# Performance work log

Hardware: AMD Instinct MI355X
Metric: run time of the kernel (lower is better)

Reference implementation:

```python
import math
import jax, jax.numpy as jnp
import numpy as np
from jax import lax

# FPN anchor layout: 1024x768 image, strides {4,8,16,32,64}, 3 anchors/location
NUM_PER_LEVEL = (147456, 36864, 9216, 2304, 576)
A_TOTAL = sum(NUM_PER_LEVEL)
BATCH = 8
PRE_NMS_TOP_N = 1000   # testing
POST_NMS_TOP_N = 1000  # testing
NMS_THRESH = 0.7
SCORE_THRESH = 0.0
MIN_SIZE = 1.0
IMG_H, IMG_W = 768.0, 1024.0
BBOX_XFORM_CLIP = math.log(1000.0 / 16.0)


def setup_inputs() -> dict:
    key = jax.random.key(0)
    k1, k2, k3, k4, k5, k6 = jax.random.split(key, 6)
    objectness = jax.random.normal(k1, (BATCH, A_TOTAL), jnp.float32)
    pred_bbox_deltas = jax.random.normal(k2, (BATCH, A_TOTAL, 4), jnp.float32) * 0.2
    # valid anchor boxes (x1, y1, x2, y2)
    cx = jax.random.uniform(k3, (A_TOTAL,), jnp.float32) * IMG_W
    cy = jax.random.uniform(k4, (A_TOTAL,), jnp.float32) * IMG_H
    w = 16.0 + jax.random.uniform(k5, (A_TOTAL,), jnp.float32) * 176.0
    h = 16.0 + jax.random.uniform(k6, (A_TOTAL,), jnp.float32) * 176.0
    anchors = jnp.stack([cx - 0.5 * w, cy - 0.5 * h, cx + 0.5 * w, cy + 0.5 * h], -1)
    return {"objectness": objectness, "pred_bbox_deltas": pred_bbox_deltas, "anchors": anchors}


def _nms_image(boxes, scores, lvl, valid):
    """batched_nms (level-offset trick) + post-NMS top-k, fixed shapes.
    boxes [K,4], scores [K], lvl [K] int, valid [K] bool -> [POST_NMS_TOP_N, 5]"""
    K = boxes.shape[0]
    s = jnp.where(valid, scores, -1.0)
    order = jnp.argsort(-s)  # decreasing score (invalid last)
    b = boxes[order]
    s = s[order]
    v = valid[order]
    # offset boxes per level so cross-level boxes never overlap (torchvision batched_nms)
    offset = lvl[order].astype(b.dtype) * (jnp.max(lax.stop_gradient(boxes)) + 1.0)
    nb = lax.stop_gradient(b) + offset[:, None]
    area = (nb[:, 2] - nb[:, 0]) * (nb[:, 3] - nb[:, 1])
    lt = jnp.maximum(nb[:, None, :2], nb[None, :, :2])  # [K,K,2]
    rb = jnp.minimum(nb[:, None, 2:], nb[None, :, 2:])
    wh = jnp.clip(rb - lt, 0.0)
    inter = wh[..., 0] * wh[..., 1]
    iou = inter / jnp.maximum(area[:, None] + area[None, :] - inter, 1e-9)
    pos = jnp.arange(K)

    def body(keep, i):
        sup = keep[i] & (iou[i] > NMS_THRESH) & (pos > i)
        return keep & ~sup, None

    keep, _ = lax.scan(body, v, pos)
    masked = jnp.where(keep, s, -1.0)
    top_s, top_i = lax.top_k(masked, POST_NMS_TOP_N)  # kept, decreasing score
    sel_b = b[top_i]
    ok = top_s > -0.5
    sel_b = jnp.where(ok[:, None], sel_b, 0.0)
    top_s = jnp.where(ok, top_s, 0.0)
    return jnp.concatenate([sel_b, top_s[:, None]], axis=-1)


def reference(objectness, pred_bbox_deltas, anchors):
    # --- box decode (BoxCoder, weights (1,1,1,1)) ---
    wa = anchors[:, 2] - anchors[:, 0]
    ha = anchors[:, 3] - anchors[:, 1]
    cxa = anchors[:, 0] + 0.5 * wa
    cya = anchors[:, 1] + 0.5 * ha
    dx, dy = pred_bbox_deltas[..., 0], pred_bbox_deltas[..., 1]
    dw = jnp.minimum(pred_bbox_deltas[..., 2], BBOX_XFORM_CLIP)
    dh = jnp.minimum(pred_bbox_deltas[..., 3], BBOX_XFORM_CLIP)
    pcx = dx * wa + cxa
    pcy = dy * ha + cya
    pw = jnp.exp(dw) * wa
    ph = jnp.exp(dh) * ha
    proposals = jnp.stack(
        [pcx - 0.5 * pw, pcy - 0.5 * ph, pcx + 0.5 * pw, pcy + 0.5 * ph], axis=-1
    )  # [B, A, 4]

    # --- per-level pre-NMS top-k (_get_top_n_idx) ---
    levels = jnp.concatenate(
        [jnp.full((n,), i, jnp.int32) for i, n in enumerate(NUM_PER_LEVEL)]
    )
    idx_parts = []
    off = 0
    for n in NUM_PER_LEVEL:
        k = min(PRE_NMS_TOP_N, n)
        _, ti = lax.top_k(objectness[:, off:off + n], k)
        idx_parts.append(ti + off)
        off += n
    top_idx = jnp.concatenate(idx_parts, axis=1)  # [B, K]

    scores = jax.nn.sigmoid(jnp.take_along_axis(objectness, top_idx, axis=1))
    lvl = levels[top_idx]
    boxes = jnp.take_along_axis(proposals, top_idx[..., None], axis=1)  # [B,K,4]

    # --- clip to image ---
    x1 = jnp.clip(boxes[..., 0], 0.0, IMG_W)
    y1 = jnp.clip(boxes[..., 1], 0.0, IMG_H)
    x2 = jnp.clip(boxes[..., 2], 0.0, IMG_W)
    y2 = jnp.clip(boxes[..., 3], 0.0, IMG_H)
    boxes = jnp.stack([x1, y1, x2, y2], axis=-1)

    # remove_small_boxes + score threshold (as validity mask; fixed shapes)
    valid = ((x2 - x1) >= MIN_SIZE) & ((y2 - y1) >= MIN_SIZE) & (scores >= SCORE_THRESH)

    # --- per-image batched NMS + post-NMS top-k ---
    return jax.vmap(_nms_image)(boxes, scores, lvl, valid)  # [B, POST_NMS_TOP_N, 5]
```

## Files before the change

kernel.cpp:

```cpp
#include <hip/hip_runtime.h>
#include <math.h>

#pragma clang fp contract(off)

#define A_TOTAL 196416
#define BATCH 8
#define KTOT 4576
#define NLEV 5
#define MSPLIT 16
#define RCAP 6144
#define NPARTS 24

static __device__ const int d_aoff[NLEV] = {0, 147456, 184320, 193536, 195840};
static __device__ const int d_n[NLEV]    = {147456, 36864, 9216, 2304, 576};
static __device__ const int d_k[NLEV]    = {1000, 1000, 1000, 1000, 576};
static __device__ const int d_spl[NLEV]  = {8, 2, 1, 1, 1};
static __device__ const int d_bp[NLEV]   = {0, 8, 10, 11, 12};
static __device__ const int d_pb_l[13]    = {0,0,0,0,0,0,0,0,1,1,2,3,4};
static __device__ const int d_pb_part[13] = {0,1,2,3,4,5,6,7,0,1,0,0,0};

#define TM_IOU (0.699999988079071044921875 + 0x1p-25)

__device__ inline unsigned int mono(float f) {
  unsigned int u = __float_as_uint(f);
  return (u & 0x80000000u) ? ~u : (u | 0x80000000u);
}
__device__ inline float imono(unsigned int m) {
  return __uint_as_float((m & 0x80000000u) ? (m & 0x7FFFFFFFu) : ~m);
}

__device__ inline int cnt_gt(const float* A, int n, float s) {
  int lo = 0, hi = n;
  while (lo < hi) { int mid = (lo + hi) >> 1; if (A[mid] > s) lo = mid + 1; else hi = mid; }
  return lo;
}
__device__ inline int cnt_ge(const float* A, int n, float s) {
  int lo = 0, hi = n;
  while (lo < hi) { int mid = (lo + hi) >> 1; if (A[mid] >= s) lo = mid + 1; else hi = mid; }
  return lo;
}

__global__ __launch_bounds__(1024) void k_hist(const float* __restrict__ obj,
                                               int* __restrict__ hist_g,
                                               int* __restrict__ cnt_g,
                                               float* __restrict__ maxblk) {
  int blk = blockIdx.x;
  int tid = threadIdx.x;
  if (blk == 0) {
    for (int i = tid; i < 40 * NPARTS; i += 1024) maxblk[i] = 0.0f;
    for (int i = tid; i < 40; i += 1024) cnt_g[i] = 0;
  }
  int b = blk / 13, pb = blk % 13;
  int l = d_pb_l[pb], part = d_pb_part[pb];
  int slice = d_n[l] / d_spl[l];
  int start = d_aoff[l] + part * slice;
  const float4* p4 = (const float4*)(obj + (size_t)b * A_TOTAL + start);
  int s4 = slice >> 2;
  __shared__ int h[4096];
  for (int i = tid; i < 4096; i += 1024) h[i] = 0;
  __syncthreads();
  for (int i = tid; i < s4; i += 1024) {
    float4 v = p4[i];
    atomicAdd(&h[mono(v.x) >> 20], 1);
    atomicAdd(&h[mono(v.y) >> 20], 1);
    atomicAdd(&h[mono(v.z) >> 20], 1);
    atomicAdd(&h[mono(v.w) >> 20], 1);
  }
  __syncthreads();
  int* outp = hist_g + (size_t)blk * 4096;
  for (int i = tid; i < 4096; i += 1024) outp[i] = h[i];
}

__global__ __launch_bounds__(1024) void k_collect(const float* __restrict__ obj,
                                                  const int* __restrict__ hist_g,
                                                  int* __restrict__ cnt_g,
                                                  unsigned long long* __restrict__ cand_g) {
  int blk = blockIdx.x;
  int b = blk / 13, pb = blk % 13;
  int l = d_pb_l[pb], part = d_pb_part[pb];
  int bl = b * NLEV + l;
  const int k = d_k[l];
  int tid = threadIdx.x;
  __shared__ int t[4096];
  __shared__ int grp[256];
  __shared__ unsigned int sP;
  __shared__ __align__(16) unsigned long long lbuf[RCAP];
  __shared__ int s_cnt, s_base;
  int parts = d_spl[l];
  const int* hb = hist_g + (size_t)(b * 13 + d_bp[l]) * 4096;
  for (int bin = tid; bin < 4096; bin += 1024) {
    int s = 0;
    for (int p = 0; p < parts; ++p) s += hb[p * 4096 + bin];
    t[bin] = s;
  }
  if (tid == 0) s_cnt = 0;
  __syncthreads();
  if (tid < 256) {
    int s = 0;
    for (int j = 0; j < 16; ++j) s += t[tid * 16 + j];
    grp[tid] = s;
  }
  __syncthreads();
  if (tid == 0) {
    int cum = 0, g, d;
    for (g = 255; g >= 0; --g) {
      if (cum + grp[g] >= k) break;
      cum += grp[g];
    }
    for (d = 15; d >= 0; --d) {
      int c = t[g * 16 + d];
      if (cum + c >= k) break;
      cum += c;
    }
    sP = (unsigned int)(g * 16 + d);
  }
  __syncthreads();
  unsigned int P = sP;
  int slice = d_n[l] / parts;
  int start = d_aoff[l] + part * slice;
  const float4* p4 = (const float4*)(obj + (size_t)b * A_TOTAL + start);
  int s4 = slice >> 2;
  int lbase = part * slice;
  for (int i = tid; i < s4; i += 1024) {
    float4 v = p4[i];
    unsigned int a[4] = {mono(v.x), mono(v.y), mono(v.z), mono(v.w)};
#pragma unroll
    for (int c = 0; c < 4; ++c) {
      if ((a[c] >> 20) >= P) {
        int slot = atomicAdd(&s_cnt, 1);
        if (slot < RCAP) {
          int idx = lbase + 4 * i + c;
          lbuf[slot] = ((unsigned long long)a[c] << 32) |
                       (unsigned int)(~(unsigned int)idx);
        }
      }
    }
  }
  __syncthreads();
  int cnt = min(s_cnt, RCAP);
  if (tid == 0) s_base = atomicAdd(&cnt_g[bl], cnt);
  __syncthreads();
  int base = s_base;
  for (int i = tid; i < cnt; i += 1024) {
    int slot = base + i;
    if (slot < RCAP) cand_g[(size_t)bl * RCAP + slot] = lbuf[i];
  }
}

__global__ __launch_bounds__(256) void k_rankdec(const unsigned long long* __restrict__ cand_g,
                                                 const int* __restrict__ cnt_g,
                                                 const float* __restrict__ deltas,
                                                 const float* __restrict__ anchors,
                                                 float* __restrict__ sc0,
                                                 float4* __restrict__ box0,
                                                 float* __restrict__ maxblk) {
  int bl = blockIdx.x / NPARTS, part = blockIdx.x % NPARTS;
  int b = bl / NLEV, l = bl % NLEV;
  const int k = d_k[l], aoff = d_aoff[l];
  int cnt = min(cnt_g[bl], RCAP);
  if (part * 256 >= cnt) return;
  __shared__ __align__(16) unsigned long long cb[RCAP];
  __shared__ unsigned int s_max;
  int tid = threadIdx.x;
  if (tid == 0) s_max = 0u;
  const unsigned long long* src = cand_g + (size_t)bl * RCAP;
  for (int i = tid; i < cnt; i += 256) cb[i] = src[i];
  __syncthreads();
  int myi = part * 256 + tid;
  float mx = 0.0f;
  if (myi < cnt) {
    unsigned long long e = cb[myi];
    int rank = 0;
    int nc2 = cnt >> 1;
    const ulonglong2* c2 = (const ulonglong2*)cb;
    for (int j = 0; j < nc2; ++j) {
      ulonglong2 v = c2[j];
      rank += (v.x > e) + (v.y > e);
    }
    if (cnt & 1) rank += (cb[cnt - 1] > e);
    if (rank < k) {
      unsigned int k32 = (unsigned int)(e >> 32);
      unsigned int idx = ~(unsigned int)(e & 0xFFFFFFFFull);
      float o = imono(k32);
      int gidx = aoff + (int)idx;
      const float* dl = deltas + ((size_t)b * A_TOTAL + gidx) * 4;
      const float* an = anchors + (size_t)gidx * 4;
      float a0 = an[0], a1 = an[1], a2 = an[2], a3 = an[3];
      float wa = a2 - a0, ha = a3 - a1;
      float cxa = a0 + 0.5f * wa, cya = a1 + 0.5f * ha;
      float dx = dl[0], dy = dl[1];
      const float CLIPV = 4.135166556742356f;
      float dw = fminf(dl[2], CLIPV), dh = fminf(dl[3], CLIPV);
      float pcx = dx * wa + cxa;
      float pcy = dy * ha + cya;
      float pw = (float)exp((double)dw) * wa;
      float ph = (float)exp((double)dh) * ha;
      float x1 = pcx - 0.5f * pw, y1 = pcy - 0.5f * ph;
      float x2 = pcx + 0.5f * pw, y2 = pcy + 0.5f * ph;
      x1 = fminf(fmaxf(x1, 0.0f), 1024.0f);
      x2 = fminf(fmaxf(x2, 0.0f), 1024.0f);
      y1 = fminf(fmaxf(y1, 0.0f), 768.0f);
      y2 = fminf(fmaxf(y2, 0.0f), 768.0f);
      float s = (float)(1.0 / (1.0 + exp(-(double)o)));
      bool valid = ((x2 - x1) >= 1.0f) && ((y2 - y1) >= 1.0f) && (s >= 0.0f);
      sc0[bl * 1024 + rank] = valid ? s : -1.0f;
      box0[bl * 1024 + rank] = make_float4(x1, y1, x2, y2);
      mx = fmaxf(fmaxf(x1, y1), fmaxf(x2, y2));
    }
  }
#pragma unroll
  for (int s = 1; s < 64; s <<= 1) mx = fmaxf(mx, __shfl_xor(mx, s));
  if ((tid & 63) == 0) atomicMax(&s_max, __float_as_uint(mx));
  __syncthreads();
  if (tid == 0) maxblk[blockIdx.x] = __uint_as_float(s_max);
}

__global__ __launch_bounds__(1024) void k_mask(const float* __restrict__ sc0,
                                               const float4* __restrict__ box0,
                                               const float* __restrict__ maxblk,
                                               float* __restrict__ lvlsc,
                                               float4* __restrict__ lvlraw,
                                               int* __restrict__ g_V,
                                               unsigned long long* __restrict__ masks) {
  int blk = blockIdx.x;
  int bl = blk / MSPLIT, part = blk % MSPLIT;
  int b = bl / NLEV, l = bl % NLEV;
  const int k = d_k[l];
  int tid = threadIdx.x, lane = tid & 63, w = tid >> 6;
  __shared__ float4 lbox[1024];
  __shared__ float s_mv;
  __shared__ int s_wcnt[16];
  if (w == 0) {
    float v = (lane < 120) ? maxblk[b * 120 + lane] : 0.0f;
    float v2 = (lane + 64 < 120) ? maxblk[b * 120 + lane + 64] : 0.0f;
    v = fmaxf(v, v2);
#pragma unroll
    for (int s = 1; s < 64; s <<= 1) v = fmaxf(v, __shfl_xor(v, s));
    if (lane == 0) s_mv = v;
  }
  bool in = tid < k;
  float s = in ? sc0[bl * 1024 + tid] : -1.0f;
  bool valid = in && (s >= 0.0f);
  unsigned long long mb = __ballot(valid);
  if (lane == 0) s_wcnt[w] = __popcll(mb);
  __syncthreads();
  int pre = 0;
  for (int ww = 0; ww < w; ++ww) pre += s_wcnt[ww];
  int j = pre + __popcll(mb & ((1ull << lane) - 1ull));
  int V = 0;
  for (int ww = 0; ww < 16; ++ww) V += s_wcnt[ww];
  float off = (float)l * (s_mv + 1.0f);
  if (valid) {
    float4 bx = box0[bl * 1024 + tid];
    lbox[j] = make_float4(bx.x + off, bx.y + off, bx.z + off, bx.w + off);
    if (part == 0) {
      lvlsc[bl * 1024 + j] = s;
      lvlraw[bl * 1024 + j] = bx;
    }
  }
  if (part == 0 && tid == 0) g_V[bl] = V;
  __syncthreads();
  int row0 = part * 64;
  if (row0 >= V) return;
  int i = row0 + lane;
  if (i >= V) return;
  float4 bb = lbox[i];
  float ba = (bb.z - bb.x) * (bb.w - bb.y);
  unsigned long long bits = 0ull;
  int jbase = w * 64;
  if (jbase + 63 > i && jbase < V) {
    int jhi = min(64, V - jbase);
    for (int jo = 0; jo < jhi; ++jo) {
      int jj = jbase + jo;
      float4 cb = lbox[jj];
      float ca = (cb.z - cb.x) * (cb.w - cb.y);
      float xx1 = fmaxf(bb.x, cb.x), yy1 = fmaxf(bb.y, cb.y);
      float xx2 = fminf(bb.z, cb.z), yy2 = fminf(bb.w, cb.w);
      float wd = fmaxf(xx2 - xx1, 0.0f), ht = fmaxf(yy2 - yy1, 0.0f);
      float inter = wd * ht;
      float denom = fmaxf(ba + ca - inter, 1e-9f);
      if ((jj > i) && ((double)inter >= TM_IOU * (double)denom)) bits |= (1ull << jo);
    }
  }
  masks[((size_t)bl * 16 + w) * 1024 + i] = bits;
}

__global__ __launch_bounds__(1024) void k_scan(const unsigned long long* __restrict__ masks,
                                               const int* __restrict__ g_V,
                                               unsigned long long* __restrict__ keepbits) {
  int bl = blockIdx.x;
  int tid = threadIdx.x, lane = tid & 63, w = tid >> 6;
  int V = g_V[bl];
  const int nch = (V + 63) / 64;
  const unsigned long long* M = masks + (size_t)bl * 16 * 1024;
  __shared__ unsigned long long s_remv[16];
  __shared__ unsigned long long s_D[2][72];
  __shared__ unsigned long long s_dw;
  if (tid < 16) s_remv[tid] = ~0ull;
  int base_w = w * 64;
  unsigned long long init_w;
  if (V <= base_w) init_w = ~0ull;
  else if (V >= base_w + 64) init_w = 0ull;
  else init_w = (~0ull) << (V - base_w);
  if (w == 0 && nch > 0) s_D[0][lane] = (lane < V) ? M[lane] : 0ull;
  if (tid < 8) { s_D[0][64 + tid] = 0ull; s_D[1][64 + tid] = 0ull; }
  unsigned long long acc = 0ull;
  __syncthreads();

  for (int c = 0; c < nch; ++c) {
    unsigned long long val = 0ull;
    int r = 64 * c + lane;
    if (w > c && w < nch && r < V) val = M[(size_t)w * 1024 + r];
    if (w == c) {
      unsigned long long red = acc;
#pragma unroll
      for (int s = 1; s < 64; s <<= 1) red |= __shfl_xor(red, s);
      unsigned long long dw = init_w | red;
      const unsigned long long* D = s_D[c & 1];
      unsigned long long pb[8];
#pragma unroll
      for (int u = 0; u < 8; ++u) pb[u] = D[u];
#pragma unroll
      for (int g = 0; g < 8; ++g) {
#pragma unroll
        for (int u = 0; u < 8; ++u) {
          int jj = g * 8 + u;
          if (!((dw >> jj) & 1ull)) dw |= pb[u];
          pb[u] = D[jj + 8];
        }
      }
      if (lane == 0) { s_dw = dw; s_remv[c] = dw; }
    }
    if (w == c + 1 && w < nch) {
      int rr = 64 * (c + 1) + lane;
      s_D[(c + 1) & 1][lane] = (rr < V) ? M[(size_t)(c + 1) * 1024 + rr] : 0ull;
    }
    __syncthreads();
    if (w > c && w < nch) {
      unsigned long long kept = ~s_dw;
      if ((kept >> lane) & 1ull) acc |= val;
    }
    __syncthreads();
  }
  if (tid < 16) keepbits[bl * 16 + tid] = ~s_remv[tid];
}

__global__ __launch_bounds__(1024) void k_out(const float* __restrict__ lvlsc,
                                              const float4* __restrict__ lvlraw,
                                              const unsigned long long* __restrict__ keepbits,
                                              const int* __restrict__ g_V,
                                              float* __restrict__ out) {
  int b = blockIdx.x;
  int tid = threadIdx.x, lane = tid & 63, wv = tid >> 6;
  __shared__ float ksc[NLEV * 1024];
  __shared__ int kj[NLEV * 1024];
  __shared__ int sK[NLEV];
  __shared__ int s_wcnt[16];
  for (int i = tid; i < 5000; i += 1024) out[(size_t)b * 5000 + i] = 0.0f;
  for (int l = 0; l < NLEV; ++l) {
    int bl = b * NLEV + l;
    int V = g_V[bl];
    bool kept = (tid < V) && ((keepbits[bl * 16 + (tid >> 6)] >> (tid & 63)) & 1ull);
    unsigned long long mb = __ballot(kept);
    if (lane == 0) s_wcnt[wv] = __popcll(mb);
    __syncthreads();
    int pre = 0;
    for (int w = 0; w < wv; ++w) pre += s_wcnt[w];
    int r = pre + __popcll(mb & ((1ull << lane) - 1ull));
    if (kept) { ksc[l * 1024 + r] = lvlsc[bl * 1024 + tid]; kj[l * 1024 + r] = tid; }
    if (tid == 0) {
      int t = 0;
      for (int w = 0; w < 16; ++w) t += s_wcnt[w];
      sK[l] = t;
    }
    __syncthreads();
  }
  int K[NLEV];
  for (int l = 0; l < NLEV; ++l) K[l] = sK[l];
  for (int l = 0; l < NLEV; ++l) {
    if (tid < K[l]) {
      float s = ksc[l * 1024 + tid];
      int rank = tid;
      for (int l2 = 0; l2 < NLEV; ++l2) {
        if (l2 == l) continue;
        const float* A = ksc + l2 * 1024;
        rank += (l2 < l) ? cnt_ge(A, K[l2], s) : cnt_gt(A, K[l2], s);
      }
      if (rank < 1000) {
        float4 bx = lvlraw[(size_t)(b * NLEV + l) * 1024 + kj[l * 1024 + tid]];
        float* op = out + (size_t)b * 5000 + (size_t)rank * 5;
        op[0] = bx.x; op[1] = bx.y; op[2] = bx.z; op[3] = bx.w; op[4] = s;
      }
    }
  }
}

extern "C" void kernel_launch(void* const* d_in, const int* in_sizes, int n_in,
                              void* d_out, int out_size, void* d_ws, size_t ws_size,
                              hipStream_t stream) {
  const float* obj     = (const float*)d_in[0];
  const float* deltas  = (const float*)d_in[1];
  const float* anchors = (const float*)d_in[2];
  float* out = (float*)d_out;

  char* p = (char*)d_ws;
  float4* box0   = (float4*)p; p += (size_t)40 * 1024 * sizeof(float4);
  float4* lvlraw = (float4*)p; p += (size_t)40 * 1024 * sizeof(float4);
  unsigned long long* cand_g   = (unsigned long long*)p; p += (size_t)40 * RCAP * 8;
  unsigned long long* masks    = (unsigned long long*)p; p += (size_t)40 * 16 * 1024 * 8;
  unsigned long long* keepbits = (unsigned long long*)p; p += (size_t)40 * 16 * 8;
  int*   hist_g = (int*)p;   p += (size_t)104 * 4096 * 4;
  int*   cnt_g  = (int*)p;   p += 40 * 4;
  float* maxblk = (float*)p; p += (size_t)40 * NPARTS * 4;
  float* sc0    = (float*)p; p += (size_t)40 * 1024 * 4;
  float* lvlsc  = (float*)p; p += (size_t)40 * 1024 * 4;
  int*   g_V    = (int*)p;   p += 40 * 4;

  hipLaunchKernelGGL(k_hist, dim3(BATCH * 13), dim3(1024), 0, stream,
                     obj, hist_g, cnt_g, maxblk);
  hipLaunchKernelGGL(k_collect, dim3(BATCH * 13), dim3(1024), 0, stream,
                     obj, hist_g, cnt_g, cand_g);
  hipLaunchKernelGGL(k_rankdec, dim3(BATCH * NLEV * NPARTS), dim3(256), 0, stream,
                     cand_g, cnt_g, deltas, anchors, sc0, box0, maxblk);
  hipLaunchKernelGGL(k_mask, dim3(BATCH * NLEV * MSPLIT), dim3(1024), 0, stream,
                     sc0, box0, maxblk, lvlsc, lvlraw, g_V, masks);
  hipLaunchKernelGGL(k_scan, dim3(BATCH * NLEV), dim3(1024), 0, stream,
                     masks, g_V, keepbits);
  hipLaunchKernelGGL(k_out, dim3(BATCH), dim3(1024), 0, stream,
                     lvlsc, lvlraw, keepbits, g_V, out);
}
```

Baseline: 207.5 us.

## Wave-aggregate candidate atomics and rebalance rank kernel to 64-thread blocks

In the candidate collection kernel, each wavefront now does one LDS atomicAdd per 4-element step, using ballot and popcount to give each lane its slot. Before, every selected candidate did its own atomic. The rank/decode kernel now runs 64-thread blocks over twice as many parts. Each thread ranks two candidates in the same shared-memory scan, which halves LDS reads per candidate and drops the block-level shared max and barrier. The catch is that each small block still stages the whole candidate list (up to 48KB of LDS), so more blocks repeat the global-to-LDS copy, and LDS use per block may limit occupancy.

```diff
diff --git a/kernel.cpp b/kernel.cpp
--- a/kernel.cpp
+++ b/kernel.cpp
@@ -9,7 +9,7 @@
 #define NLEV 5
 #define MSPLIT 16
 #define RCAP 6144
-#define NPARTS 24
+#define NPARTS 48
 
 static __device__ const int d_aoff[NLEV] = {0, 147456, 184320, 193536, 195840};
 static __device__ const int d_n[NLEV]    = {147456, 36864, 9216, 2304, 576};
@@ -80,7 +80,7 @@
   int l = d_pb_l[pb], part = d_pb_part[pb];
   int bl = b * NLEV + l;
   const int k = d_k[l];
-  int tid = threadIdx.x;
+  int tid = threadIdx.x, lane = tid & 63;
   __shared__ int t[4096];
   __shared__ int grp[256];
   __shared__ unsigned int sP;
@@ -126,12 +126,19 @@
     unsigned int a[4] = {mono(v.x), mono(v.y), mono(v.z), mono(v.w)};
 #pragma unroll
     for (int c = 0; c < 4; ++c) {
-      if ((a[c] >> 20) >= P) {
-        int slot = atomicAdd(&s_cnt, 1);
-        if (slot < RCAP) {
-          int idx = lbase + 4 * i + c;
-          lbuf[slot] = ((unsigned long long)a[c] << 32) |
-                       (unsigned int)(~(unsigned int)idx);
+      bool q = (a[c] >> 20) >= P;
+      unsigned long long mb = __ballot(q);
+      if (mb) {
+        int base;
+        if (lane == 0) base = atomicAdd(&s_cnt, __popcll(mb));
+        base = __shfl(base, 0);
+        if (q) {
+          int slot = base + __popcll(mb & ((1ull << lane) - 1ull));
+          if (slot < RCAP) {
+            int idx = lbase + 4 * i + c;
+            lbuf[slot] = ((unsigned long long)a[c] << 32) |
+                         (unsigned int)(~(unsigned int)idx);
+          }
         }
       }
     }
@@ -147,72 +154,88 @@
   }
 }
 
-__global__ __launch_bounds__(256) void k_rankdec(const unsigned long long* __restrict__ cand_g,
-                                                 const int* __restrict__ cnt_g,
-                                                 const float* __restrict__ deltas,
-                                                 const float* __restrict__ anchors,
-                                                 float* __restrict__ sc0,
-                                                 float4* __restrict__ box0,
-                                                 float* __restrict__ maxblk) {
+__device__ inline float decode_emit(unsigned long long e, int rank, int b,
+                                    int k, int aoff, int bl,
+                                    const float* __restrict__ deltas,
+                                    const float* __restrict__ anchors,
+                                    float* __restrict__ sc0,
+                                    float4* __restrict__ box0) {
+  if (rank >= k) return 0.0f;
+  unsigned int k32 = (unsigned int)(e >> 32);
+  unsigned int idx = ~(unsigned int)(e & 0xFFFFFFFFull);
+  float o = imono(k32);
+  int gidx = aoff + (int)idx;
+  const float* dl = deltas + ((size_t)b * A_TOTAL + gidx) * 4;
+  const float* an = anchors + (size_t)gidx * 4;
+  float a0 = an[0], a1 = an[1], a2 = an[2], a3 = an[3];
+  float wa = a2 - a0, ha = a3 - a1;
+  float cxa = a0 + 0.5f * wa, cya = a1 + 0.5f * ha;
+  float dx = dl[0], dy = dl[1];
+  const float CLIPV = 4.135166556742356f;
+  float dw = fminf(dl[2], CLIPV), dh = fminf(dl[3], CLIPV);
+  float pcx = dx * wa + cxa;
+  float pcy = dy * ha + cya;
+  float pw = (float)exp((double)dw) * wa;
+  float ph = (float)exp((double)dh) * ha;
+  float x1 = pcx - 0.5f * pw, y1 = pcy - 0.5f * ph;
+  float x2 = pcx + 0.5f * pw, y2 = pcy + 0.5f * ph;
+  x1 = fminf(fmaxf(x1, 0.0f), 1024.0f);
+  x2 = fminf(fmaxf(x2, 0.0f), 1024.0f);
+  y1 = fminf(fmaxf(y1, 0.0f), 768.0f);
+  y2 = fminf(fmaxf(y2, 0.0f), 768.0f);
+  float s = (float)(1.0 / (1.0 + exp(-(double)o)));
+  bool valid = ((x2 - x1) >= 1.0f) && ((y2 - y1) >= 1.0f) && (s >= 0.0f);
+  sc0[bl * 1024 + rank] = valid ? s : -1.0f;
+  box0[bl * 1024 + rank] = make_float4(x1, y1, x2, y2);
+  return fmaxf(fmaxf(x1, y1), fmaxf(x2, y2));
+}
+
+__global__ __launch_bounds__(64) void k_rankdec(const unsigned long long* __restrict__ cand_g,
+                                                const int* __restrict__ cnt_g,
+                                                const float* __restrict__ deltas,
+                                                const float* __restrict__ anchors,
+                                                float* __restrict__ sc0,
+                                                float4* __restrict__ box0,
+                                                float* __restrict__ maxblk) {
   int bl = blockIdx.x / NPARTS, part = blockIdx.x % NPARTS;
   int b = bl / NLEV, l = bl % NLEV;
   const int k = d_k[l], aoff = d_aoff[l];
   int cnt = min(cnt_g[bl], RCAP);
-  if (part * 256 >= cnt) return;
+  if (part * 128 >= cnt) return;
   __shared__ __align__(16) unsigned long long cb[RCAP];
-  __shared__ unsigned int s_max;
   int tid = threadIdx.x;
-  if (tid == 0) s_max = 0u;
   const unsigned long long* src = cand_g + (size_t)bl * RCAP;
-  for (int i = tid; i < cnt; i += 256) cb[i] = src[i];
-  __syncthreads();
-  int myi = part * 256 + tid;
+  {
+    const ulonglong2* s2 = (const ulonglong2*)src;
+    ulonglong2* d2 = (ulonglong2*)cb;
+    int n2 = cnt >> 1;
+    for (int i = tid; i < n2; i += 64) d2[i] = s2[i];
+    if ((cnt & 1) && tid == 0) cb[cnt - 1] = src[cnt - 1];
+  }
+  __syncthreads();
+  int i0 = part * 128 + tid, i1 = i0 + 64;
+  unsigned long long e0 = ~0ull, e1 = ~0ull;
+  if (i0 < cnt) e0 = cb[i0];
+  if (i1 < cnt) e1 = cb[i1];
+  int r0 = 0, r1 = 0;
+  int nc2 = cnt >> 1;
+  const ulonglong2* c2 = (const ulonglong2*)cb;
+  for (int j = 0; j < nc2; ++j) {
+    ulonglong2 v = c2[j];
+    r0 += (v.x > e0) + (v.y > e0);
+    r1 += (v.x > e1) + (v.y > e1);
+  }
+  if (cnt & 1) {
+    unsigned long long v = cb[cnt - 1];
+    r0 += (v > e0);
+    r1 += (v > e1);
+  }
   float mx = 0.0f;
-  if (myi < cnt) {
-    unsigned long long e = cb[myi];
-    int rank = 0;
-    int nc2 = cnt >> 1;
-    const ulonglong2* c2 = (const ulonglong2*)cb;
-    for (int j = 0; j < nc2; ++j) {
-      ulonglong2 v = c2[j];
-      rank += (v.x > e) + (v.y > e);
-    }
-    if (cnt & 1) rank += (cb[cnt - 1] > e);
-    if (rank < k) {
-      unsigned int k32 = (unsigned int)(e >> 32);
-      unsigned int idx = ~(unsigned int)(e & 0xFFFFFFFFull);
-      float o = imono(k32);
-      int gidx = aoff + (int)idx;
-      const float* dl = deltas + ((size_t)b * A_TOTAL + gidx) * 4;
-      const float* an = anchors + (size_t)gidx * 4;
-      float a0 = an[0], a1 = an[1], a2 = an[2], a3 = an[3];
-      float wa = a2 - a0, ha = a3 - a1;
-      float cxa = a0 + 0.5f * wa, cya = a1 + 0.5f * ha;
-      float dx = dl[0], dy = dl[1];
-      const float CLIPV = 4.135166556742356f;
-      float dw = fminf(dl[2], CLIPV), dh = fminf(dl[3], CLIPV);
-      float pcx = dx * wa + cxa;
-      float pcy = dy * ha + cya;
-      float pw = (float)exp((double)dw) * wa;
-      float ph = (float)exp((double)dh) * ha;
-      float x1 = pcx - 0.5f * pw, y1 = pcy - 0.5f * ph;
-      float x2 = pcx + 0.5f * pw, y2 = pcy + 0.5f * ph;
-      x1 = fminf(fmaxf(x1, 0.0f), 1024.0f);
-      x2 = fminf(fmaxf(x2, 0.0f), 1024.0f);
-      y1 = fminf(fmaxf(y1, 0.0f), 768.0f);
-      y2 = fminf(fmaxf(y2, 0.0f), 768.0f);
-      float s = (float)(1.0 / (1.0 + exp(-(double)o)));
-      bool valid = ((x2 - x1) >= 1.0f) && ((y2 - y1) >= 1.0f) && (s >= 0.0f);
-      sc0[bl * 1024 + rank] = valid ? s : -1.0f;
-      box0[bl * 1024 + rank] = make_float4(x1, y1, x2, y2);
-      mx = fmaxf(fmaxf(x1, y1), fmaxf(x2, y2));
-    }
-  }
+  if (i0 < cnt) mx = fmaxf(mx, decode_emit(e0, r0, b, k, aoff, bl, deltas, anchors, sc0, box0));
+  if (i1 < cnt) mx = fmaxf(mx, decode_emit(e1, r1, b, k, aoff, bl, deltas, anchors, sc0, box0));
 #pragma unroll
   for (int s = 1; s < 64; s <<= 1) mx = fmaxf(mx, __shfl_xor(mx, s));
-  if ((tid & 63) == 0) atomicMax(&s_max, __float_as_uint(mx));
-  __syncthreads();
-  if (tid == 0) maxblk[blockIdx.x] = __uint_as_float(s_max);
+  if (tid == 0) maxblk[blockIdx.x] = mx;
 }
 
 __global__ __launch_bounds__(1024) void k_mask(const float* __restrict__ sc0,
@@ -231,9 +254,9 @@
   __shared__ float s_mv;
   __shared__ int s_wcnt[16];
   if (w == 0) {
-    float v = (lane < 120) ? maxblk[b * 120 + lane] : 0.0f;
-    float v2 = (lane + 64 < 120) ? maxblk[b * 120 + lane + 64] : 0.0f;
-    v = fmaxf(v, v2);
+    float v = 0.0f;
+    for (int i = lane; i < NLEV * NPARTS; i += 64)
+      v = fmaxf(v, maxblk[b * (NLEV * NPARTS) + i]);
 #pragma unroll
     for (int s = 1; s < 64; s <<= 1) v = fmaxf(v, __shfl_xor(v, s));
     if (lane == 0) s_mv = v;
@@ -420,7 +443,7 @@
                      obj, hist_g, cnt_g, maxblk);
   hipLaunchKernelGGL(k_collect, dim3(BATCH * 13), dim3(1024), 0, stream,
                      obj, hist_g, cnt_g, cand_g);
-  hipLaunchKernelGGL(k_rankdec, dim3(BATCH * NLEV * NPARTS), dim3(256), 0, stream,
+  hipLaunchKernelGGL(k_rankdec, dim3(BATCH * NLEV * NPARTS), dim3(64), 0, stream,
                      cand_g, cnt_g, deltas, anchors, sc0, box0, maxblk);
   hipLaunchKernelGGL(k_mask, dim3(BATCH * NLEV * MSPLIT), dim3(1024), 0, stream,
                      sc0, box0, maxblk, lvlsc, lvlraw, g_V, masks);
```

Measured after the change: 214.7 us. 1.03x slower.
